# Optimization experiments

Measured on AMD Instinct MI355X. Metric: run time of the kernel, lower is better.

Reference implementation:

```python
import jax, jax.numpy as jnp
import numpy as np


def setup_inputs() -> dict:
    key = jax.random.key(0)
    k1, k2 = jax.random.split(key)
    B, N, E, D = 8, 2048, 64, 128
    spatial_embedding = jax.random.normal(k1, (B, N, E), dtype=jnp.float32)
    z = jax.random.normal(k2, (B, N, D), dtype=jnp.float32)
    return {"spatial_embedding": spatial_embedding, "z": z}


def reference(spatial_embedding, z):
    # Pairwise squared L2 distance via ||a||^2 + ||b||^2 - 2 a.b
    # (same math as (e0-e1).norm(2,-1)**2, avoids [B,N,N,E] intermediate)
    sq = jnp.sum(spatial_embedding * spatial_embedding, axis=-1)  # [B,N]
    inner = jnp.einsum('bie,bje->bij', spatial_embedding, spatial_embedding)
    d2 = jnp.maximum(sq[:, :, None] + sq[:, None, :] - 2.0 * inner, 0.0)  # [B,N,N]
    sim = jnp.exp(-d2)
    attn = sim / jnp.sum(sim, axis=-1, keepdims=True)
    out = jnp.einsum('bij,bjd->bid', attn, z)
    return out
```

## Files before the change

### kernel.cpp

```cpp
#include <hip/hip_runtime.h>
#include <hip/hip_bf16.h>

#define BB 8
#define NN 2048
#define EE 64
#define DD 128
#define BN (BB * NN)

typedef __attribute__((ext_vector_type(8))) short short8v;
typedef __attribute__((ext_vector_type(4))) float float4v;

__device__ __forceinline__ short f2bf(float f) {
    __hip_bfloat16 h = __float2bfloat16(f);
    return *reinterpret_cast<short*>(&h);
}
__device__ __forceinline__ uint32_t pack2bf(float a, float b) {
    return (uint32_t)(uint16_t)f2bf(a) | ((uint32_t)(uint16_t)f2bf(b) << 16);
}

#define GLD16(gp, lp)                                                          \
    __builtin_amdgcn_global_load_lds(                                          \
        (const __attribute__((address_space(1))) void*)(gp),                   \
        (__attribute__((address_space(3))) void*)(lp), 16, 0, 0)
#define GLD4(gp, lp)                                                           \
    __builtin_amdgcn_global_load_lds(                                          \
        (const __attribute__((address_space(1))) void*)(gp),                   \
        (__attribute__((address_space(3))) void*)(lp), 4, 0, 0)

__global__ __launch_bounds__(256) void prep_kernel(const float* __restrict__ emb,
                                                   const float* __restrict__ z,
                                                   short* __restrict__ embq,
                                                   short* __restrict__ zq,
                                                   float* __restrict__ sq) {
    __shared__ float zl[64 * 129];
    const int bid = blockIdx.x;
    const int t = threadIdx.x;

    if (bid < 512) {
        int gid = bid * 256 + t;
        int s = gid & 63;
        int ke = (gid >> 6) & 1;
        int r16 = (gid >> 7) & 127;
        int b = gid >> 14;
        int i = r16 * 16 + (s & 15);
        int e0 = ke * 32 + ((s >> 4) & 3) * 8;
        const float4* src = reinterpret_cast<const float4*>(emb + ((size_t)(b * NN + i)) * EE + e0);
        float4 v0 = src[0], v1 = src[1];
        short8v o;
        o[0] = f2bf(v0.x); o[1] = f2bf(v0.y); o[2] = f2bf(v0.z); o[3] = f2bf(v0.w);
        o[4] = f2bf(v1.x); o[5] = f2bf(v1.y); o[6] = f2bf(v1.z); o[7] = f2bf(v1.w);
        *reinterpret_cast<short8v*>(embq + (size_t)gid * 8) = o;
    } else if (bid < 768) {
        int v = bid - 512;
        int b = v >> 5;
        int jt = v & 31;
        int jb = jt * 64;
#pragma unroll
        for (int k = 0; k < 8; ++k) {
            int idx = t + k * 256;
            int jl = idx >> 5, c4 = idx & 31;
            float4 w = reinterpret_cast<const float4*>(z + ((size_t)(b * NN + jb + jl)) * DD)[c4];
            float* p = &zl[jl * 129 + c4 * 4];
            p[0] = w.x; p[1] = w.y; p[2] = w.z; p[3] = w.w;
        }
        __syncthreads();
#pragma unroll
        for (int k = 0; k < 4; ++k) {
            int sid = t + k * 256;
            int blk = sid >> 6, s = sid & 63;
            int ktl = blk >> 3, nt = blk & 7;
            int d = nt * 16 + (s & 15);
            int jl = ktl * 32 + ((s >> 4) & 3) * 8;
            short8v o;
#pragma unroll
            for (int e = 0; e < 8; ++e) o[e] = f2bf(zl[(jl + e) * 129 + d]);
            *reinterpret_cast<short8v*>(zq + ((size_t)((b * 64 + jt * 2 + ktl) * 8 + nt) * 64 + s) * 8) = o;
        }
    } else {
        int v = bid - 768;
        int q = t & 15;
#pragma unroll
        for (int p = 0; p < 4; ++p) {
            int row = v * 64 + p * 16 + (t >> 4);
            float4 rv = reinterpret_cast<const float4*>(emb + (size_t)row * EE)[q];
            float a0 = __bfloat162float(__float2bfloat16(rv.x));
            float a1 = __bfloat162float(__float2bfloat16(rv.y));
            float a2 = __bfloat162float(__float2bfloat16(rv.z));
            float a3 = __bfloat162float(__float2bfloat16(rv.w));
            float s2 = a0 * a0 + a1 * a1 + a2 * a2 + a3 * a3;
#pragma unroll
            for (int off = 1; off < 16; off <<= 1) s2 += __shfl_xor(s2, off);
            if (q == 0) sq[row] = s2;
        }
    }
}

__global__ __launch_bounds__(256, 2) void attn_mfma(const short* __restrict__ embq,
                                                    const short* __restrict__ zq,
                                                    const float* __restrict__ sq,
                                                    float* __restrict__ outnum,
                                                    float* __restrict__ den,
                                                    int njs) {
    __shared__ short sU[4][2048];
    __shared__ int4 sEmbJ[2][512];
    __shared__ float sSqJ[2][64];

    const int t = threadIdx.x;
    const int bid = blockIdx.x;
    const int b = bid & 7;
    const int q = bid >> 3;
    const int it = q & 15;
    const int js = q >> 4;
    const int ib = it * 128;
    const int w = t >> 6;
    const int l = t & 63;
    const int g = (l >> 4) & 3;
    const int c = l & 15;

    const int4* embqI4 = (const int4*)embq;
    const short8v* zq8 = (const short8v*)zq;
    const float* sqB = sq + b * NN;

    const int ntiles = 32 / njs;
    const int jt0 = js * ntiles;
    const int jtEnd = jt0 + ntiles;

    int4* sUi = (int4*)&sU[0][0];

    {
        const int4* srcI = embqI4 + (size_t)(b * 128 + it * 8) * 2 * 64;
#pragma unroll
        for (int k = 0; k < 4; ++k) GLD16(srcI + t + k * 256, sUi + t + k * 256);
        const int4* srcJ = embqI4 + (size_t)(b * 128 + jt0 * 4) * 2 * 64;
        GLD16(srcJ + t, &sEmbJ[0][t]);
        GLD16(srcJ + t + 256, &sEmbJ[0][t + 256]);
        if (t < 64) GLD4(sqB + jt0 * 64 + t, &sSqJ[0][t]);
    }
    __syncthreads();

    short8v qkB[2][2];
#pragma unroll
    for (int m = 0; m < 2; ++m)
#pragma unroll
        for (int ke = 0; ke < 2; ++ke)
            qkB[m][ke] = *reinterpret_cast<const short8v*>(&sUi[((w * 2 + m) * 2 + ke) * 64 + l]);
    float sqi[2];
#pragma unroll
    for (int m = 0; m < 2; ++m) sqi[m] = sqB[ib + w * 32 + m * 16 + c];

    float dsum[2] = {0.f, 0.f};
    float4v acc[2][8];
#pragma unroll
    for (int m = 0; m < 2; ++m)
#pragma unroll
        for (int nt = 0; nt < 8; ++nt) acc[m][nt] = (float4v){0.f, 0.f, 0.f, 0.f};

    char* ptw = (char*)&sU[w][0];
    const int swz = (c & 7) << 4;

    int cur = 0;
    for (int jt = jt0; jt < jtEnd; ++jt, cur ^= 1) {
        {
            int jn = (jt + 1 < jtEnd) ? jt + 1 : jt;
            int nxt = cur ^ 1;
            const int4* srcJ = embqI4 + (size_t)(b * 128 + jn * 4) * 2 * 64;
            GLD16(srcJ + t, &sEmbJ[nxt][t]);
            GLD16(srcJ + t + 256, &sEmbJ[nxt][t + 256]);
            if (t < 64) GLD4(sqB + jn * 64 + t, &sSqJ[nxt][t]);
        }

        uint32_t pk[2][4][2];
        float d2min = 1e30f;
#pragma unroll
        for (int J = 0; J < 4; ++J) {
            short8v afrag[2];
            afrag[0] = *reinterpret_cast<const short8v*>(&sEmbJ[cur][(J * 2 + 0) * 64 + l]);
            afrag[1] = *reinterpret_cast<const short8v*>(&sEmbJ[cur][(J * 2 + 1) * 64 + l]);
#pragma unroll
            for (int m = 0; m < 2; ++m) {
                float4v sfr = (float4v){0.f, 0.f, 0.f, 0.f};
                sfr = __builtin_amdgcn_mfma_f32_16x16x32_bf16(afrag[0], qkB[m][0], sfr, 0, 0, 0);
                sfr = __builtin_amdgcn_mfma_f32_16x16x32_bf16(afrag[1], qkB[m][1], sfr, 0, 0, 0);
                float pw[4];
#pragma unroll
                for (int r = 0; r < 4; ++r) {
                    float d2 = fmaxf(sqi[m] + sSqJ[cur][J * 16 + 4 * g + r] - 2.0f * sfr[r], 0.0f);
                    d2min = fminf(d2min, d2);
                    pw[r] = __expf(-d2);
                    dsum[m] += pw[r];
                }
                pk[m][J][0] = pack2bf(pw[0], pw[1]);
                pk[m][J][1] = pack2bf(pw[2], pw[3]);
            }
        }

        if (!__all(d2min > 13.8f)) {
#pragma unroll
            for (int m = 0; m < 2; ++m) {
                const int woff = (m * 2048 + c * 128 + g * 8) ^ swz;
#pragma unroll
                for (int J = 0; J < 4; ++J)
                    *reinterpret_cast<unsigned long long*>(ptw + (woff ^ (J * 32))) =
                        (unsigned long long)pk[m][J][0] | ((unsigned long long)pk[m][J][1] << 32);
            }
            short8v pa[2][2];
#pragma unroll
            for (int m = 0; m < 2; ++m)
#pragma unroll
                for (int kt = 0; kt < 2; ++kt)
                    pa[m][kt] = *reinterpret_cast<const short8v*>(
                        ptw + ((m * 2048 + c * 128 + kt * 64 + g * 16) ^ swz));
#pragma unroll
            for (int nt = 0; nt < 8; ++nt) {
                short8v z0 = zq8[(size_t)((b * 64 + jt * 2 + 0) * 8 + nt) * 64 + l];
                short8v z1 = zq8[(size_t)((b * 64 + jt * 2 + 1) * 8 + nt) * 64 + l];
#pragma unroll
                for (int m = 0; m < 2; ++m) {
                    acc[m][nt] = __builtin_amdgcn_mfma_f32_16x16x32_bf16(pa[m][0], z0, acc[m][nt], 0, 0, 0);
                    acc[m][nt] = __builtin_amdgcn_mfma_f32_16x16x32_bf16(pa[m][1], z1, acc[m][nt], 0, 0, 0);
                }
            }
        }

        __syncthreads();
    }

#pragma unroll
    for (int m = 0; m < 2; ++m) {
        dsum[m] += __shfl_xor(dsum[m], 16);
        dsum[m] += __shfl_xor(dsum[m], 32);
    }

    if (njs == 1) {
#pragma unroll
        for (int m = 0; m < 2; ++m) {
            float invr[4];
#pragma unroll
            for (int r = 0; r < 4; ++r) invr[r] = 1.0f / __shfl(dsum[m], 4 * g + r);
#pragma unroll
            for (int r = 0; r < 4; ++r) {
                size_t row = (size_t)(b * NN + ib + w * 32 + m * 16 + 4 * g + r);
#pragma unroll
                for (int nt = 0; nt < 8; ++nt)
                    outnum[row * DD + nt * 16 + c] = acc[m][nt][r] * invr[r];
            }
        }
    } else {
        if (l < 16) {
            den[(size_t)js * BN + b * NN + ib + w * 32 + l] = dsum[0];
            den[(size_t)js * BN + b * NN + ib + w * 32 + 16 + l] = dsum[1];
        }
        if (!__all(fmaxf(dsum[0], dsum[1]) < 1e-6f)) {
#pragma unroll
            for (int m = 0; m < 2; ++m)
#pragma unroll
                for (int r = 0; r < 4; ++r) {
                    size_t row = (size_t)js * BN + b * NN + ib + w * 32 + m * 16 + 4 * g + r;
#pragma unroll
                    for (int nt = 0; nt < 8; ++nt)
                        outnum[row * DD + nt * 16 + c] = acc[m][nt][r];
                }
        }
    }
}

__global__ __launch_bounds__(256) void reduce_kernel(const float4* __restrict__ num,
                                                     const float* __restrict__ den,
                                                     float4* __restrict__ out,
                                                     int njs) {
    int i4 = blockIdx.x * 256 + threadIdx.x;
    int row = i4 >> 5;
    float4 ns = make_float4(0.f, 0.f, 0.f, 0.f);
    float ds = 0.f;
    for (int js = 0; js < njs; ++js) {
        float dj = den[(size_t)js * BN + row];
        ds += dj;
        if (dj >= 1e-6f) {
            float4 v = num[(size_t)js * ((size_t)BN * (DD / 4)) + i4];
            ns.x += v.x; ns.y += v.y; ns.z += v.z; ns.w += v.w;
        }
    }
    float inv = 1.0f / ds;
    out[i4] = make_float4(ns.x * inv, ns.y * inv, ns.z * inv, ns.w * inv);
}

extern "C" void kernel_launch(void* const* d_in, const int* in_sizes, int n_in,
                              void* d_out, int out_size, void* d_ws, size_t ws_size,
                              hipStream_t stream) {
    (void)in_sizes; (void)n_in; (void)out_size;
    const float* emb = (const float*)d_in[0];
    const float* z = (const float*)d_in[1];
    float* out = (float*)d_out;
    float* ws = (float*)d_ws;

    int njs = 1;
    if (ws_size >= 40ull * 1024 * 1024) njs = 4;
    else if (ws_size >= 24ull * 1024 * 1024) njs = 2;

    float* sqw = ws;
    float* denw = ws + BN;
    float* numw = denw + (size_t)njs * BN;
    size_t numFloats = (njs > 1) ? (size_t)njs * BN * DD : 0;
    short* embqw = (short*)(numw + numFloats);
    short* zqw = embqw + (size_t)BB * NN * EE;

    prep_kernel<<<1024, 256, 0, stream>>>(emb, z, embqw, zqw, sqw);

    attn_mfma<<<8 * 16 * njs, 256, 0, stream>>>(embqw, zqw, sqw,
                                                njs == 1 ? out : numw, denw, njs);

    if (njs > 1) {
        reduce_kernel<<<(BN * (DD / 4)) / 256, 256, 0, stream>>>(
            (const float4*)numw, denw, (float4*)out, njs);
    }
}
```

Baseline: 35.94 us.

## Triple-stage J-tile prefetch with vmcnt waits and skip exp for dead sub-tiles

Prefetches two J tiles ahead, using explicit vmcnt waits and raw barriers in place of __syncthreads. Each wave now keeps its own copy of the sq values so they can be read as a float4. The d2 values are computed first, and exp is evaluated only when the whole tile, and then the individual 16-column sub-block, has some distance below the cutoff. Dead sub-blocks are written as zeros. This cuts exp work and load latency but adds register pressure from the d2 array and relies on precise vmcnt counting.

```diff
diff --git a/kernel.cpp b/kernel.cpp
--- a/kernel.cpp
+++ b/kernel.cpp
@@ -103,7 +103,7 @@
                                                     int njs) {
     __shared__ short sU[4][2048];
     __shared__ int4 sEmbJ[2][512];
-    __shared__ float sSqJ[2][64];
+    __shared__ float sSqJ[2][4][64];
 
     const int t = threadIdx.x;
     const int bid = blockIdx.x;
@@ -127,16 +127,24 @@
 
     int4* sUi = (int4*)&sU[0][0];
 
+#define STAGE(buf, tile)                                                       \
+    do {                                                                       \
+        const int4* _sj = embqI4 + (size_t)(b * 128 + (tile) * 4) * 2 * 64;    \
+        GLD16(_sj + t, &sEmbJ[buf][t]);                                        \
+        GLD16(_sj + t + 256, &sEmbJ[buf][t + 256]);                            \
+        GLD4(sqB + (tile) * 64 + l, &sSqJ[buf][w][0]);                         \
+    } while (0)
+
     {
         const int4* srcI = embqI4 + (size_t)(b * 128 + it * 8) * 2 * 64;
 #pragma unroll
         for (int k = 0; k < 4; ++k) GLD16(srcI + t + k * 256, sUi + t + k * 256);
-        const int4* srcJ = embqI4 + (size_t)(b * 128 + jt0 * 4) * 2 * 64;
-        GLD16(srcJ + t, &sEmbJ[0][t]);
-        GLD16(srcJ + t + 256, &sEmbJ[0][t + 256]);
-        if (t < 64) GLD4(sqB + jt0 * 64 + t, &sSqJ[0][t]);
-    }
-    __syncthreads();
+    }
+    STAGE(0, jt0);
+    STAGE(1, jt0 + 1);
+    asm volatile("s_waitcnt vmcnt(3)" ::: "memory");
+    __builtin_amdgcn_s_barrier();
+    __builtin_amdgcn_sched_barrier(0);
 
     short8v qkB[2][2];
 #pragma unroll
@@ -160,48 +168,49 @@
 
     int cur = 0;
     for (int jt = jt0; jt < jtEnd; ++jt, cur ^= 1) {
-        {
-            int jn = (jt + 1 < jtEnd) ? jt + 1 : jt;
-            int nxt = cur ^ 1;
-            const int4* srcJ = embqI4 + (size_t)(b * 128 + jn * 4) * 2 * 64;
-            GLD16(srcJ + t, &sEmbJ[nxt][t]);
-            GLD16(srcJ + t + 256, &sEmbJ[nxt][t + 256]);
-            if (t < 64) GLD4(sqB + jn * 64 + t, &sSqJ[nxt][t]);
-        }
-
-        uint32_t pk[2][4][2];
-        float d2min = 1e30f;
+        float d2v[2][4][4];
+        float d2minJ[4];
 #pragma unroll
         for (int J = 0; J < 4; ++J) {
-            short8v afrag[2];
-            afrag[0] = *reinterpret_cast<const short8v*>(&sEmbJ[cur][(J * 2 + 0) * 64 + l]);
-            afrag[1] = *reinterpret_cast<const short8v*>(&sEmbJ[cur][(J * 2 + 1) * 64 + l]);
+            short8v a0 = *reinterpret_cast<const short8v*>(&sEmbJ[cur][(J * 2 + 0) * 64 + l]);
+            short8v a1 = *reinterpret_cast<const short8v*>(&sEmbJ[cur][(J * 2 + 1) * 64 + l]);
+            float4 sqj = *reinterpret_cast<const float4*>(&sSqJ[cur][w][J * 16 + 4 * g]);
+            float mn = 1e30f;
 #pragma unroll
             for (int m = 0; m < 2; ++m) {
                 float4v sfr = (float4v){0.f, 0.f, 0.f, 0.f};
-                sfr = __builtin_amdgcn_mfma_f32_16x16x32_bf16(afrag[0], qkB[m][0], sfr, 0, 0, 0);
-                sfr = __builtin_amdgcn_mfma_f32_16x16x32_bf16(afrag[1], qkB[m][1], sfr, 0, 0, 0);
-                float pw[4];
-#pragma unroll
-                for (int r = 0; r < 4; ++r) {
-                    float d2 = fmaxf(sqi[m] + sSqJ[cur][J * 16 + 4 * g + r] - 2.0f * sfr[r], 0.0f);
-                    d2min = fminf(d2min, d2);
-                    pw[r] = __expf(-d2);
-                    dsum[m] += pw[r];
+                sfr = __builtin_amdgcn_mfma_f32_16x16x32_bf16(a0, qkB[m][0], sfr, 0, 0, 0);
+                sfr = __builtin_amdgcn_mfma_f32_16x16x32_bf16(a1, qkB[m][1], sfr, 0, 0, 0);
+                d2v[m][J][0] = fmaxf(fmaf(-2.0f, sfr[0], sqi[m] + sqj.x), 0.0f);
+                d2v[m][J][1] = fmaxf(fmaf(-2.0f, sfr[1], sqi[m] + sqj.y), 0.0f);
+                d2v[m][J][2] = fmaxf(fmaf(-2.0f, sfr[2], sqi[m] + sqj.z), 0.0f);
+                d2v[m][J][3] = fmaxf(fmaf(-2.0f, sfr[3], sqi[m] + sqj.w), 0.0f);
+                mn = fminf(mn, fminf(fminf(d2v[m][J][0], d2v[m][J][1]),
+                                     fminf(d2v[m][J][2], d2v[m][J][3])));
+            }
+            d2minJ[J] = mn;
+        }
+        float tmin = fminf(fminf(d2minJ[0], d2minJ[1]), fminf(d2minJ[2], d2minJ[3]));
+
+        if (!__all(tmin > 13.8f)) {
+#pragma unroll
+            for (int J = 0; J < 4; ++J) {
+                const bool live = !__all(d2minJ[J] > 13.8f);
+#pragma unroll
+                for (int m = 0; m < 2; ++m) {
+                    unsigned long long pword = 0ull;
+                    if (live) {
+                        float p0 = __expf(-d2v[m][J][0]);
+                        float p1 = __expf(-d2v[m][J][1]);
+                        float p2 = __expf(-d2v[m][J][2]);
+                        float p3 = __expf(-d2v[m][J][3]);
+                        dsum[m] += (p0 + p1) + (p2 + p3);
+                        pword = (unsigned long long)pack2bf(p0, p1) |
+                                ((unsigned long long)pack2bf(p2, p3) << 32);
+                    }
+                    *reinterpret_cast<unsigned long long*>(
+                        ptw + ((m * 2048 + c * 128 + g * 8) ^ swz ^ (J * 32))) = pword;
                 }
-                pk[m][J][0] = pack2bf(pw[0], pw[1]);
-                pk[m][J][1] = pack2bf(pw[2], pw[3]);
-            }
-        }
-
-        if (!__all(d2min > 13.8f)) {
-#pragma unroll
-            for (int m = 0; m < 2; ++m) {
-                const int woff = (m * 2048 + c * 128 + g * 8) ^ swz;
-#pragma unroll
-                for (int J = 0; J < 4; ++J)
-                    *reinterpret_cast<unsigned long long*>(ptw + (woff ^ (J * 32))) =
-                        (unsigned long long)pk[m][J][0] | ((unsigned long long)pk[m][J][1] << 32);
             }
             short8v pa[2][2];
 #pragma unroll
@@ -222,8 +231,17 @@
             }
         }
 
-        __syncthreads();
-    }
+        __builtin_amdgcn_s_barrier();
+        if (jt + 2 < jtEnd) {
+            STAGE(cur, jt + 2);
+            asm volatile("s_waitcnt vmcnt(3)" ::: "memory");
+        } else {
+            asm volatile("s_waitcnt vmcnt(0)" ::: "memory");
+        }
+        __builtin_amdgcn_s_barrier();
+        __builtin_amdgcn_sched_barrier(0);
+    }
+#undef STAGE
 
 #pragma unroll
     for (int m = 0; m < 2; ++m) {
```

Result: faster. 30.98 us (-13.8%).
